# Kernel tuning notes

Hardware: AMD Instinct MI355X
Metric: run time of the kernel (lower is better)

The kernel has to match this reference:

```python
import jax, jax.numpy as jnp
import numpy as np

B, L, D = 2, 2048, 1024
H = 16
HD = D // H  # 64
WINDOW = 256


def setup_inputs() -> dict:
    key = jax.random.key(0)
    k1, k2, k3 = jax.random.split(key, 3)
    s = 0.02
    return {
        "x": jax.random.normal(k1, (B, L, D), dtype=jnp.float32),
        "w_qkv": jax.random.normal(k2, (D, 3 * D), dtype=jnp.float32) * s,
        "b_qkv": jnp.zeros((3 * D,), dtype=jnp.float32),
        "w_out": jax.random.normal(k3, (D, D), dtype=jnp.float32) * s,
        "b_out": jnp.zeros((D,), dtype=jnp.float32),
    }


def _window_mask(seq_len, window_size, dtype):
    # row i allows cols in [i - w//2, i + w//2] inclusive (symmetric band)
    half = window_size // 2
    i = jnp.arange(seq_len)[:, None]
    j = jnp.arange(seq_len)[None, :]
    allowed = jnp.abs(i - j) <= half
    return jnp.where(allowed, jnp.zeros((), dtype), jnp.asarray(-jnp.inf, dtype))


def reference(x, w_qkv, b_qkv, w_out, b_out):
    b, l, d = x.shape
    qkv = x @ w_qkv + b_qkv                        # [B, L, 3D]
    qkv = qkv.reshape(b, l, 3, H, HD)
    q = jnp.transpose(qkv[:, :, 0], (0, 2, 1, 3))   # [B, H, L, HD]
    k = jnp.transpose(qkv[:, :, 1], (0, 2, 1, 3))
    v = jnp.transpose(qkv[:, :, 2], (0, 2, 1, 3))
    scale = 1.0 / np.sqrt(HD)
    scores = jnp.einsum("bhqd,bhkd->bhqk", q, k) * scale
    scores = scores + _window_mask(l, WINDOW, scores.dtype)[None, None]
    attn = jax.nn.softmax(scores, axis=-1)          # dropout: eval mode (p applied only in training)
    out = jnp.einsum("bhqk,bhkd->bhqd", attn, v)    # [B, H, L, HD]
    out = jnp.transpose(out, (0, 2, 1, 3)).reshape(b, l, d)
    return out @ w_out + b_out
```

## Files before the change

kernel.cpp:

```cpp
#include <hip/hip_runtime.h>
#include <math.h>

#define B_    2
#define L_    2048
#define D_    1024
#define H_    16
#define HD_   64
#define HALF_ 128
#define TQ    32
#define PST   296

typedef __attribute__((ext_vector_type(8))) short short8;
typedef __attribute__((ext_vector_type(4))) float f32x4;

__device__ __forceinline__ unsigned short f2bf(float x) {
  unsigned int u = __float_as_uint(x);
  u = (u + 0x7fffu + ((u >> 16) & 1u)) >> 16;
  return (unsigned short)u;
}

__device__ __forceinline__ void async_cp16(const unsigned short* g, unsigned short* l) {
  __builtin_amdgcn_global_load_lds(
      (const __attribute__((address_space(1))) unsigned int*)g,
      (__attribute__((address_space(3))) unsigned int*)l, 16, 0, 0);
}

__device__ __forceinline__ void tr_round32(const float* __restrict__ in,
                                           unsigned short* __restrict__ hi,
                                           int N, int K, int n0, int k0,
                                           float (*t)[33], int tid) {
  {
    const int kl = tid >> 3, nl = (tid & 7) * 4;
    const float4 v = *(const float4*)&in[(size_t)(k0 + kl) * N + n0 + nl];
    t[kl][nl + 0] = v.x; t[kl][nl + 1] = v.y;
    t[kl][nl + 2] = v.z; t[kl][nl + 3] = v.w;
  }
  __syncthreads();
  {
    const int no = tid >> 3, ko = (tid & 7) * 4;
    ushort4 h;
    h.x = f2bf(t[ko + 0][no]);
    h.y = f2bf(t[ko + 1][no]);
    h.z = f2bf(t[ko + 2][no]);
    h.w = f2bf(t[ko + 3][no]);
    *(ushort4*)&hi[(size_t)(n0 + no) * K + k0 + ko] = h;
  }
}

__global__ __launch_bounds__(256) void prep(const float* __restrict__ x,
                                            unsigned short* __restrict__ x_hi,
                                            const float* __restrict__ w_qkv,
                                            unsigned short* __restrict__ wqkvT,
                                            const float* __restrict__ w_out,
                                            unsigned short* __restrict__ woutT) {
  __shared__ float t[32][33];
  const int bx = blockIdx.x, tid = threadIdx.x;
  if (bx < 4096) {
    const int i = (bx * 256 + tid) * 4;
    const float4 a = *(const float4*)&x[i];
    ushort4 h;
    h.x = f2bf(a.x); h.y = f2bf(a.y); h.z = f2bf(a.z); h.w = f2bf(a.w);
    *(ushort4*)&x_hi[i] = h;
  } else if (bx < 7168) {
    const int tb = bx - 4096;
    tr_round32(w_qkv, wqkvT, 3 * D_, D_, (tb % 96) * 32, (tb / 96) * 32, t, tid);
  } else {
    const int tb = bx - 7168;
    tr_round32(w_out, woutT, D_, D_, (tb % 32) * 32, (tb / 32) * 32, t, tid);
  }
}

__global__ __launch_bounds__(256, 3) void gemm_qkv(
    const unsigned short* __restrict__ Ah,
    const unsigned short* __restrict__ Bh,
    const float* __restrict__ bias,
    unsigned short* __restrict__ q_hi,
    unsigned short* __restrict__ kT,
    unsigned short* __restrict__ vTile,
    int N, int K) {
  __shared__ char smraw[33792];
  const int tid  = threadIdx.x;
  const int wave = tid >> 6, lane = tid & 63;

  const int lin = blockIdx.y * gridDim.x + blockIdx.x;
  const int swz = (lin & 7) * 96 + (lin >> 3);
  const int n0 = (swz % 24) * 128, m0 = (swz / 24) * 128;

  const int wm = (wave >> 1) * 64, wn = (wave & 1) * 64;
  const int quad = lane >> 4, ln16 = lane & 15;

  const bool isA = wave < 2;
  const unsigned short* src = isA ? Ah : Bh;
  const int baserow = isA ? m0 : n0;
  const int instbase = (wave & 1) * 8;
  const int dbase = (isA ? 0 : 16384) + instbase * 1024;
  size_t goff[8];
#pragma unroll
  for (int i = 0; i < 8; ++i) {
    const int r = (instbase + i) * 8 + (lane >> 3);
    const int c = (lane & 7) ^ (r & 7);
    goff[i] = (size_t)(baserow + r) * K + c * 8;
  }

  int offA[4], offB[4];
#pragma unroll
  for (int t = 0; t < 4; ++t) {
    const int r = wm + t * 16 + ln16;
    offA[t] = r * 128 + ((quad ^ (r & 7)) * 16);
    const int rn = wn + t * 16 + ln16;
    offB[t] = 16384 + rn * 128 + ((quad ^ (rn & 7)) * 16);
  }

  f32x4 acc[4][4] = {};
  const char* smb = (const char*)smraw;

  for (int k0 = 0; k0 < K; k0 += 64) {
#pragma unroll
    for (int i = 0; i < 8; ++i)
      async_cp16(src + goff[i] + k0,
                 (unsigned short*)(smraw + dbase + i * 1024));
    __syncthreads();

    {
      short8 ah[4], bh[4];
#pragma unroll
      for (int t = 0; t < 4; ++t) {
        ah[t] = *(const short8*)(smb + offA[t]);
        bh[t] = *(const short8*)(smb + offB[t]);
      }
#pragma unroll
      for (int t = 0; t < 4; ++t)
#pragma unroll
        for (int u = 0; u < 4; ++u)
          acc[t][u] = __builtin_amdgcn_mfma_f32_16x16x32_bf16(bh[u], ah[t], acc[t][u], 0, 0, 0);
    }
    {
      short8 ah[4], bh[4];
#pragma unroll
      for (int t = 0; t < 4; ++t) {
        ah[t] = *(const short8*)(smb + (offA[t] ^ 64));
        bh[t] = *(const short8*)(smb + (offB[t] ^ 64));
      }
#pragma unroll
      for (int t = 0; t < 4; ++t)
#pragma unroll
        for (int u = 0; u < 4; ++u)
          acc[t][u] = __builtin_amdgcn_mfma_f32_16x16x32_bf16(bh[u], ah[t], acc[t][u], 0, 0, 0);
    }
    __syncthreads();
  }

  const int slot = n0 >> 10;
  const int nbase = n0 & 1023;

  if (slot == 0) {
#pragma unroll
    for (int t = 0; t < 4; ++t) {
      const int m = m0 + wm + t * 16 + ln16;
#pragma unroll
      for (int u = 0; u < 4; ++u) {
        const int nl = wn + u * 16 + quad * 4;
        const float4 bq = *(const float4*)&bias[n0 + nl];
        ushort4 h;
        h.x = f2bf(acc[t][u][0] + bq.x);
        h.y = f2bf(acc[t][u][1] + bq.y);
        h.z = f2bf(acc[t][u][2] + bq.z);
        h.w = f2bf(acc[t][u][3] + bq.w);
        *(ushort4*)&q_hi[(size_t)m * 1024 + nbase + nl] = h;
      }
    }
  } else if (slot == 1) {
#pragma unroll
    for (int t = 0; t < 4; ++t) {
      const int tok = m0 + wm + t * 16 + ln16;
      const int bb = tok >> 11, j = tok & 2047;
#pragma unroll
      for (int u = 0; u < 4; ++u) {
        const int nl = wn + u * 16 + quad * 4;
        const float4 bq = *(const float4*)&bias[n0 + nl];
        const int hd = nbase + nl;
        const int hh_ = hd >> 6, dg = (hd & 63) >> 3, di = hd & 7;
        ushort4 h;
        h.x = f2bf(acc[t][u][0] + bq.x);
        h.y = f2bf(acc[t][u][1] + bq.y);
        h.z = f2bf(acc[t][u][2] + bq.z);
        h.w = f2bf(acc[t][u][3] + bq.w);
        const size_t o =
            ((((size_t)bb * 16 + hh_) * 8 + dg) * 2048 + j) * 8 + di;
        *(ushort4*)&kT[o] = h;
      }
    }
  } else {
    unsigned short* lt = (unsigned short*)smraw;
#pragma unroll
    for (int t = 0; t < 4; ++t) {
      const int ml = wm + t * 16 + ln16;
#pragma unroll
      for (int u = 0; u < 4; ++u) {
        const int nl = wn + u * 16 + quad * 4;
        const float4 bq = *(const float4*)&bias[n0 + nl];
        ushort4 h;
        h.x = f2bf(acc[t][u][0] + bq.x);
        h.y = f2bf(acc[t][u][1] + bq.y);
        h.z = f2bf(acc[t][u][2] + bq.z);
        h.w = f2bf(acc[t][u][3] + bq.w);
        *(ushort4*)&lt[ml * 132 + nl] = h;
      }
    }
    __syncthreads();
    const int jg0 = (m0 & 2047) >> 3;
    const int bb = m0 >> 11;
#pragma unroll
    for (int it = 0; it < 8; ++it) {
      const int chunk = it * 256 + tid;
      const int hd = chunk & 127, tokg = chunk >> 7;
      short8 hh;
#pragma unroll
      for (int s = 0; s < 8; ++s)
        hh[s] = (short)lt[(tokg * 8 + s) * 132 + hd];
      const size_t o =
          (((size_t)bb * 256 + jg0 + tokg) * 1024 + nbase + hd) * 8;
      *(short8*)&vTile[o] = hh;
    }
  }
}

template <int EPI>
__global__ __launch_bounds__(256) void gemm_n64s(const unsigned short* __restrict__ Ah,
                                                 const unsigned short* __restrict__ Bh,
                                                 const float* __restrict__ bias,
                                                 float* __restrict__ C,
                                                 unsigned short* __restrict__ vTile,
                                                 int N, int K) {
  __shared__ unsigned short sm[6144];
  const int tid  = threadIdx.x;
  const int wave = tid >> 6, lane = tid & 63;
  const int m0 = blockIdx.y * 128, n0 = blockIdx.x * 64;
  const int quad = lane >> 4, ln16 = lane & 15;
  const int wm = wave * 32;

  const unsigned short* sptr[3];
  int dstoff[3];
#pragma unroll
  for (int s = 0; s < 3; ++s) {
    const int g = wave * 3 + s;
    const bool isA = g < 8;
    const unsigned short* base = isA ? Ah : Bh;
    const int r0 = isA ? (m0 + g * 16) : (n0 + (g - 8) * 16);
    const int r = r0 + (lane >> 2);
    const int q = (lane & 3) ^ ((r >> 1) & 3);
    sptr[s] = base + (size_t)r * K + q * 8;
    dstoff[s] = isA ? g * 1024 : 8192 + (g - 8) * 1024;
  }

  int offA[2], offB[4];
#pragma unroll
  for (int t = 0; t < 2; ++t) {
    const int r = wm + t * 16 + ln16;
    offA[t] = r * 64 + ((quad ^ ((r >> 1) & 3)) * 16);
  }
#pragma unroll
  for (int u = 0; u < 4; ++u) {
    const int rn = u * 16 + ln16;
    offB[u] = rn * 64 + ((quad ^ ((rn >> 1) & 3)) * 16);
  }

  f32x4 acc[2][4] = {};
  const char* smb = (const char*)sm;

  for (int k0 = 0; k0 < K; k0 += 32) {
#pragma unroll
    for (int s = 0; s < 3; ++s)
      async_cp16(sptr[s] + k0, (unsigned short*)((char*)sm + dstoff[s]));
    __syncthreads();

    short8 ah[2], bh[4];
#pragma unroll
    for (int t = 0; t < 2; ++t) ah[t] = *(const short8*)(smb + offA[t]);
#pragma unroll
    for (int u = 0; u < 4; ++u) bh[u] = *(const short8*)(smb + 8192 + offB[u]);
#pragma unroll
    for (int t = 0; t < 2; ++t)
#pragma unroll
      for (int u = 0; u < 4; ++u)
        acc[t][u] = __builtin_amdgcn_mfma_f32_16x16x32_bf16(ah[t], bh[u], acc[t][u], 0, 0, 0);
    __syncthreads();
  }

#pragma unroll
  for (int u = 0; u < 4; ++u) {
    const int col = n0 + u * 16 + ln16;
    const float bv = bias[col];
#pragma unroll
    for (int t = 0; t < 2; ++t) {
      const int row0 = m0 + wm + t * 16 + quad * 4;
      if (EPI == 0) {
#pragma unroll
        for (int e = 0; e < 4; ++e)
          C[(size_t)(row0 + e) * N + col] = acc[t][u][e] + bv;
      } else {
        const int bb = row0 >> 11, l0 = row0 & 2047;
        ushort4 vh;
        vh.x = f2bf(acc[t][u][0] + bv);
        vh.y = f2bf(acc[t][u][1] + bv);
        vh.z = f2bf(acc[t][u][2] + bv);
        vh.w = f2bf(acc[t][u][3] + bv);
        const size_t o =
            (((size_t)bb * 256 + (l0 >> 3)) * 1024 + col) * 8 + (l0 & 7);
        *(ushort4*)&vTile[o] = vh;
      }
    }
  }
}

__global__ __launch_bounds__(256, 4) void attn_mfma(
    const unsigned short* __restrict__ q_hi,
    const unsigned short* __restrict__ kT,
    const unsigned short* __restrict__ vTile,
    unsigned short* __restrict__ attn_h) {
  __shared__ unsigned short P[TQ * PST];
  __shared__ float redS[2][32];

  const int b   = blockIdx.z;
  const int h   = blockIdx.y;
  const int i0  = blockIdx.x * TQ;
  const int tid = threadIdx.x;
  const int wave = tid >> 6, lane = tid & 63;
  const int quad = lane >> 4, ln16 = lane & 15;
  const int mt = wave >> 1, np = wave & 1;
  const int jlo = i0 - HALF_;
  const int rbase = mt * 16 + quad * 4;

  float s[4] = {0.f, 0.f, 0.f, 0.f};
  {
    const size_t qbase =
        (size_t)(b * L_ + i0 + mt * 16 + ln16) * 1024 + h * 64 + quad * 8;
    const short8 qh0 = *(const short8*)&q_hi[qbase];
    const short8 qh1 = *(const short8*)&q_hi[qbase + 32];

    const size_t kb0 = (((size_t)b * 16 + h) * 8 + quad) * 2048 * 8;
    const size_t kb1 = (((size_t)b * 16 + h) * 8 + quad + 4) * 2048 * 8;

#pragma unroll
    for (int c = 0; c < 9; ++c) {
      const int nt   = np + 2 * c;
      const int jabs = jlo + nt * 16 + ln16;
      const int jcl  = min(max(jabs, 0), L_ - 1);
      const short8 kh0 = *(const short8*)&kT[kb0 + (size_t)jcl * 8];
      const short8 kh1 = *(const short8*)&kT[kb1 + (size_t)jcl * 8];

      f32x4 a = {};
      a = __builtin_amdgcn_mfma_f32_16x16x32_bf16(qh0, kh0, a, 0, 0, 0);
      a = __builtin_amdgcn_mfma_f32_16x16x32_bf16(qh1, kh1, a, 0, 0, 0);

      const int colj = nt * 16 + ln16;
#pragma unroll
      for (int e = 0; e < 4; ++e) {
        const int iabs = i0 + rbase + e;
        const bool ok = (jabs >= 0) && (jabs < L_) && (abs(iabs - jabs) <= HALF_);
        const float ev = ok ? __expf(a[e] * 0.125f) : 0.f;
        s[e] += ev;
        P[(rbase + e) * PST + colj] = f2bf(ev);
      }
    }
  }
#pragma unroll
  for (int e = 0; e < 4; ++e) {
    s[e] += __shfl_xor(s[e], 1);
    s[e] += __shfl_xor(s[e], 2);
    s[e] += __shfl_xor(s[e], 4);
    s[e] += __shfl_xor(s[e], 8);
  }
  if (ln16 == 0) {
#pragma unroll
    for (int e = 0; e < 4; ++e) redS[np][rbase + e] = s[e];
  }
  __syncthreads();
  float rinv[4];
#pragma unroll
  for (int e = 0; e < 4; ++e) rinv[e] = 1.f / (s[e] + redS[np ^ 1][rbase + e]);

  f32x4 o[2] = {};
  {
    const int dp = np;
    const char* pb = (const char*)P;
#pragma unroll
    for (int c = 0; c < 9; ++c) {
      const short8 pf =
          *(const short8*)(pb + (mt * 16 + ln16) * (PST * 2) + c * 64 + quad * 16);
      int j0 = jlo + c * 32 + quad * 8;
      j0 = min(max(j0, 0), L_ - 8);
      const size_t jgbase = ((size_t)b * 256 + (j0 >> 3)) * 1024;
#pragma unroll
      for (int t = 0; t < 2; ++t) {
        const size_t vb = (jgbase + (h * 64 + dp * 32 + t * 16 + ln16)) * 8;
        const short8 vh = *(const short8*)&vTile[vb];
        o[t] = __builtin_amdgcn_mfma_f32_16x16x32_bf16(pf, vh, o[t], 0, 0, 0);
      }
    }
  }

  __syncthreads();
  float* ob = (float*)P;
  {
    const int dp = np;
#pragma unroll
    for (int t = 0; t < 2; ++t)
#pragma unroll
      for (int e = 0; e < 4; ++e)
        ob[(rbase + e) * 68 + dp * 32 + t * 16 + ln16] = o[t][e] * rinv[e];
  }
  __syncthreads();
  {
    const int rr = tid >> 3, ck = tid & 7;
    const float* rp = ob + rr * 68 + ck * 8;
    const float4 f0 = *(const float4*)&rp[0];
    const float4 f1 = *(const float4*)&rp[4];
    short8 hh;
    hh[0] = (short)f2bf(f0.x); hh[1] = (short)f2bf(f0.y);
    hh[2] = (short)f2bf(f0.z); hh[3] = (short)f2bf(f0.w);
    hh[4] = (short)f2bf(f1.x); hh[5] = (short)f2bf(f1.y);
    hh[6] = (short)f2bf(f1.z); hh[7] = (short)f2bf(f1.w);
    const size_t oo = ((size_t)(b * L_ + i0 + rr)) * 1024 + h * 64 + ck * 8;
    *(short8*)&attn_h[oo] = hh;
  }
}

extern "C" void kernel_launch(void* const* d_in, const int* in_sizes, int n_in,
                              void* d_out, int out_size, void* d_ws, size_t ws_size,
                              hipStream_t stream) {
  const float* x     = (const float*)d_in[0];
  const float* w_qkv = (const float*)d_in[1];
  const float* b_qkv = (const float*)d_in[2];
  const float* w_out = (const float*)d_in[3];
  const float* b_out = (const float*)d_in[4];
  float* out = (float*)d_out;

  const int M = B_ * L_;

  char* ws = (char*)d_ws;
  unsigned short* x_hi    = (unsigned short*)(ws + 0);
  unsigned short* wqkvT   = (unsigned short*)(ws + 16777216);
  unsigned short* woutT   = (unsigned short*)(ws + 23068672);
  unsigned short* q_hi    = (unsigned short*)(ws + 25165824);
  unsigned short* kT      = (unsigned short*)(ws + 33554432);
  unsigned short* vTile   = (unsigned short*)(ws + 41943040);
  unsigned short* attn_hi = (unsigned short*)(ws + 0);

  prep<<<8192, 256, 0, stream>>>(x, x_hi, w_qkv, wqkvT, w_out, woutT);
  {
    dim3 g(3072 / 128, M / 128);
    gemm_qkv<<<g, 256, 0, stream>>>(x_hi, wqkvT, b_qkv, q_hi, kT, vTile,
                                    3072, D_);
  }
  {
    dim3 g(L_ / TQ, H_, B_);
    attn_mfma<<<g, 256, 0, stream>>>(q_hi, kT, vTile, attn_hi);
  }
  {
    dim3 g(D_ / 64, M / 128);
    gemm_n64s<0><<<g, 256, 0, stream>>>(attn_hi, woutT, b_out, out,
                                        nullptr, D_, D_);
  }
}
```

Baseline: 161.7 us.

## Rework output GEMM with K=64 steps, block swizzle, and vectorized stores

Replaces the output-projection GEMM with a version that loads 64-wide K slices per iteration, which halves the number of barrier-synchronized iterations, and uses an 8-way XOR swizzle in LDS. It remaps block indices so neighbouring blocks share A/B tiles in cache. It also swaps the MFMA operand order so each lane holds 4 consecutive output columns, enabling float4 bias loads and float4 stores. LDS use per block grows, and a launch bound of 2 blocks per SM is added, which may cap occupancy.

```diff
diff --git a/kernel.cpp b/kernel.cpp
--- a/kernel.cpp
+++ b/kernel.cpp
@@ -225,90 +225,98 @@
   }
 }
 
-template <int EPI>
-__global__ __launch_bounds__(256) void gemm_n64s(const unsigned short* __restrict__ Ah,
-                                                 const unsigned short* __restrict__ Bh,
-                                                 const float* __restrict__ bias,
-                                                 float* __restrict__ C,
-                                                 unsigned short* __restrict__ vTile,
-                                                 int N, int K) {
-  __shared__ unsigned short sm[6144];
+__global__ __launch_bounds__(256, 2) void gemm_out(
+    const unsigned short* __restrict__ Ah,
+    const unsigned short* __restrict__ Bh,
+    const float* __restrict__ bias,
+    float* __restrict__ C,
+    int N, int K) {
+  __shared__ char smraw[24576];
   const int tid  = threadIdx.x;
   const int wave = tid >> 6, lane = tid & 63;
-  const int m0 = blockIdx.y * 128, n0 = blockIdx.x * 64;
+
+  const int lin = blockIdx.y * gridDim.x + blockIdx.x;
+  const int swz = (lin & 7) * 64 + (lin >> 3);
+  const int n0 = (swz % 16) * 64, m0 = (swz / 16) * 128;
+
   const int quad = lane >> 4, ln16 = lane & 15;
   const int wm = wave * 32;
 
-  const unsigned short* sptr[3];
-  int dstoff[3];
-#pragma unroll
-  for (int s = 0; s < 3; ++s) {
-    const int g = wave * 3 + s;
-    const bool isA = g < 8;
+  const unsigned short* sptr[6];
+  int dstoff[6];
+#pragma unroll
+  for (int s = 0; s < 6; ++s) {
+    const int g = wave * 6 + s;
+    const bool isA = g < 16;
     const unsigned short* base = isA ? Ah : Bh;
-    const int r0 = isA ? (m0 + g * 16) : (n0 + (g - 8) * 16);
-    const int r = r0 + (lane >> 2);
-    const int q = (lane & 3) ^ ((r >> 1) & 3);
-    sptr[s] = base + (size_t)r * K + q * 8;
-    dstoff[s] = isA ? g * 1024 : 8192 + (g - 8) * 1024;
+    const int r0 = isA ? g * 8 : (g - 16) * 8;
+    const int r = r0 + (lane >> 3);
+    const int c = (lane & 7) ^ (r & 7);
+    sptr[s] = base + (size_t)((isA ? m0 : n0) + r) * K + c * 8;
+    dstoff[s] = isA ? g * 1024 : 16384 + (g - 16) * 1024;
   }
 
   int offA[2], offB[4];
 #pragma unroll
   for (int t = 0; t < 2; ++t) {
     const int r = wm + t * 16 + ln16;
-    offA[t] = r * 64 + ((quad ^ ((r >> 1) & 3)) * 16);
+    offA[t] = r * 128 + ((quad ^ (r & 7)) * 16);
   }
 #pragma unroll
   for (int u = 0; u < 4; ++u) {
     const int rn = u * 16 + ln16;
-    offB[u] = rn * 64 + ((quad ^ ((rn >> 1) & 3)) * 16);
+    offB[u] = 16384 + rn * 128 + ((quad ^ (rn & 7)) * 16);
   }
 
   f32x4 acc[2][4] = {};
-  const char* smb = (const char*)sm;
-
-  for (int k0 = 0; k0 < K; k0 += 32) {
-#pragma unroll
-    for (int s = 0; s < 3; ++s)
-      async_cp16(sptr[s] + k0, (unsigned short*)((char*)sm + dstoff[s]));
+  const char* smb = (const char*)smraw;
+
+  for (int k0 = 0; k0 < K; k0 += 64) {
+#pragma unroll
+    for (int s = 0; s < 6; ++s)
+      async_cp16(sptr[s] + k0, (unsigned short*)(smraw + dstoff[s]));
     __syncthreads();
 
-    short8 ah[2], bh[4];
-#pragma unroll
-    for (int t = 0; t < 2; ++t) ah[t] = *(const short8*)(smb + offA[t]);
-#pragma unroll
-    for (int u = 0; u < 4; ++u) bh[u] = *(const short8*)(smb + 8192 + offB[u]);
-#pragma unroll
-    for (int t = 0; t < 2; ++t)
-#pragma unroll
-      for (int u = 0; u < 4; ++u)
-        acc[t][u] = __builtin_amdgcn_mfma_f32_16x16x32_bf16(ah[t], bh[u], acc[t][u], 0, 0, 0);
+    {
+      short8 ah[2], bh[4];
+#pragma unroll
+      for (int t = 0; t < 2; ++t) ah[t] = *(const short8*)(smb + offA[t]);
+#pragma unroll
+      for (int u = 0; u < 4; ++u) bh[u] = *(const short8*)(smb + offB[u]);
+#pragma unroll
+      for (int t = 0; t < 2; ++t)
+#pragma unroll
+        for (int u = 0; u < 4; ++u)
+          acc[t][u] = __builtin_amdgcn_mfma_f32_16x16x32_bf16(bh[u], ah[t], acc[t][u], 0, 0, 0);
+    }
+    {
+      short8 ah[2], bh[4];
+#pragma unroll
+      for (int t = 0; t < 2; ++t) ah[t] = *(const short8*)(smb + (offA[t] ^ 64));
+#pragma unroll
+      for (int u = 0; u < 4; ++u) bh[u] = *(const short8*)(smb + (offB[u] ^ 64));
+#pragma unroll
+      for (int t = 0; t < 2; ++t)
+#pragma unroll
+        for (int u = 0; u < 4; ++u)
+          acc[t][u] = __builtin_amdgcn_mfma_f32_16x16x32_bf16(bh[u], ah[t], acc[t][u], 0, 0, 0);
+    }
     __syncthreads();
   }
 
 #pragma unroll
-  for (int u = 0; u < 4; ++u) {
-    const int col = n0 + u * 16 + ln16;
-    const float bv = bias[col];
-#pragma unroll
-    for (int t = 0; t < 2; ++t) {
-      const int row0 = m0 + wm + t * 16 + quad * 4;
-      if (EPI == 0) {
-#pragma unroll
-        for (int e = 0; e < 4; ++e)
-          C[(size_t)(row0 + e) * N + col] = acc[t][u][e] + bv;
-      } else {
-        const int bb = row0 >> 11, l0 = row0 & 2047;
-        ushort4 vh;
-        vh.x = f2bf(acc[t][u][0] + bv);
-        vh.y = f2bf(acc[t][u][1] + bv);
-        vh.z = f2bf(acc[t][u][2] + bv);
-        vh.w = f2bf(acc[t][u][3] + bv);
-        const size_t o =
-            (((size_t)bb * 256 + (l0 >> 3)) * 1024 + col) * 8 + (l0 & 7);
-        *(ushort4*)&vTile[o] = vh;
-      }
+  for (int t = 0; t < 2; ++t) {
+    const int m = m0 + wm + t * 16 + ln16;
+#pragma unroll
+    for (int u = 0; u < 4; ++u) {
+      const int n = n0 + u * 16 + quad * 4;
+      const float4 bq = *(const float4*)&bias[n];
+      float4 o;
+      o.x = acc[t][u][0] + bq.x;
+      o.y = acc[t][u][1] + bq.y;
+      o.z = acc[t][u][2] + bq.z;
+      o.w = acc[t][u][3] + bq.w;
+      *(float4*)&C[(size_t)m * N + n] = o;
     }
   }
 }
@@ -459,7 +467,6 @@
   }
   {
     dim3 g(D_ / 64, M / 128);
-    gemm_n64s<0><<<g, 256, 0, stream>>>(attn_hi, woutT, b_out, out,
-                                        nullptr, D_, D_);
-  }
-}
+    gemm_out<<<g, 256, 0, stream>>>(attn_hi, woutT, b_out, out, D_, D_);
+  }
+}
```

Result: no change. 158.8 us (-1.8%).
